# Kernel tuning notes

Measured on AMD Instinct MI355X. Metric: run time of the kernel, lower is better.

The kernel has to match this reference:

```python
import jax, jax.numpy as jnp
import numpy as np

FEW_SHOT_K = 5
NUM_CLASSES = 3
SUPPORT_SIZE = 100


def setup_inputs() -> dict:
    key = jax.random.key(0)
    ks = jax.random.split(key, 12)
    B, S, H = 64, 512, 1024
    scale = 0.02
    return {
        "hidden_states": jax.random.normal(ks[0], (B, S, H), jnp.float32),
        "labels": jax.random.randint(ks[1], (B,), 0, NUM_CLASSES),
        "support_features": jax.random.normal(ks[2], (SUPPORT_SIZE, H), jnp.float32),
        "support_labels": jax.random.randint(ks[3], (SUPPORT_SIZE,), 0, NUM_CLASSES),
        "W_sim": jax.random.normal(ks[4], (128, H), jnp.float32) * scale,
        "b_sim": jnp.zeros((128,), jnp.float32),
        "W_div": jax.random.normal(ks[5], (128, H), jnp.float32) * scale,
        "b_div": jnp.zeros((128,), jnp.float32),
        "W_meta": jax.random.normal(ks[6], (H, H), jnp.float32) * scale,
        "b_meta": jnp.zeros((H,), jnp.float32),
        "W_con": jax.random.normal(ks[7], (256, H), jnp.float32) * scale,
        "b_con": jnp.zeros((256,), jnp.float32),
    }


def reference(hidden_states, labels, support_features, support_labels,
              W_sim, b_sim, W_div, b_div, W_meta, b_meta, W_con, b_con):
    B, S, H = hidden_states.shape
    pooled = hidden_states.mean(axis=1)                       # [B,H] sentence/query features
    similarity_features = pooled @ W_sim.T + b_sim            # [B,128]
    diversity_features = pooled @ W_div.T + b_div             # [B,128]
    meta = jnp.einsum('bsh,oh->bso', hidden_states, W_meta) + b_meta  # [B,S,H]
    meta_contrastive = meta.mean(axis=1) @ W_con.T + b_con    # [B,256]

    # update_support_set: circular buffer write starting at ptr=0, B<100 -> plain slice.
    # Features are .detach()'d in torch before storage.
    supF = support_features.at[:B].set(jax.lax.stop_gradient(pooled))
    supL = support_labels.at[:B].set(labels)

    # topk similarity + softmax weights
    sims = pooled @ supF.T                                    # [B,100]
    top_v, top_i = jax.lax.top_k(sims, FEW_SHOT_K)            # [B,K]
    weights = jax.nn.softmax(top_v, axis=1)                   # [B,K]
    sel_labels = supL[top_i]                                  # [B,K]

    # vectorized replacement of the per-element python scatter loop:
    # pred[b,c] = sum_i weights[b,i] * [sel_labels[b,i] == c], 0<=label<3 guard
    # jax.nn.one_hot yields all-zeros for out-of-range labels, matching the guard.
    onehot = jax.nn.one_hot(sel_labels, NUM_CLASSES, dtype=weights.dtype)  # [B,K,3]
    pred = jnp.einsum('bkc,bk->bc', onehot, weights)          # [B,3]
    few_shot_predictions = jnp.broadcast_to(pred[:, None, :], (B, S, NUM_CLASSES))

    return few_shot_predictions, similarity_features, diversity_features, meta_contrastive
```

## Files before the change

### kernel.cpp

```cpp
#include <hip/hip_runtime.h>

#define BB 64
#define SS 512
#define HH 1024
#define SUP 100
#define KFS 5
#define NCLS 3
#define SEG 32
#define KSPLIT 8
#define KB (HH / KSPLIT)
#define KC 32
#define ASLD 68

__global__ void pool_partial(const float* __restrict__ hs, float* __restrict__ part) {
    int blk = blockIdx.x;
    int b   = blk >> 5;
    int seg = blk & (SEG - 1);
    int t   = threadIdx.x;
    const float4* src = (const float4*)(hs + (size_t)b * SS * HH);
    float4 acc = make_float4(0.f, 0.f, 0.f, 0.f);
    int s0 = seg * (SS / SEG);
#pragma unroll
    for (int s = s0; s < s0 + (SS / SEG); ++s) {
        float4 v = src[s * 256 + t];
        acc.x += v.x; acc.y += v.y; acc.z += v.z; acc.w += v.w;
    }
    ((float4*)part)[(seg * BB + b) * 256 + t] = acc;
}

__global__ void pool_reduce(const float* __restrict__ part, float* __restrict__ pooled) {
    int b = blockIdx.x;
    int t = threadIdx.x;
    float4 acc = make_float4(0.f, 0.f, 0.f, 0.f);
    for (int seg = 0; seg < SEG; ++seg) {
        float4 v = ((const float4*)part)[(seg * BB + b) * 256 + t];
        acc.x += v.x; acc.y += v.y; acc.z += v.z; acc.w += v.w;
    }
    const float inv = 1.0f / 512.0f;
    acc.x *= inv; acc.y *= inv; acc.z *= inv; acc.w *= inv;
    ((float4*)pooled)[b * 256 + t] = acc;
}

__device__ __forceinline__ void gemm64_partial(const float* __restrict__ A,
                                               const float* __restrict__ W,
                                               float* __restrict__ partOut, int N,
                                               int n0, int k0, int ks, int t,
                                               float (*As)[ASLD], float (*Bs)[ASLD]) {
    int tm = t >> 4, tn = t & 15;
    int lr = t >> 2, lq = t & 3;
    float acc[4][4] = {};
    for (int kc = 0; kc < KB; kc += KC) {
        int ka = k0 + kc + lq * 4;
        float4 a0 = *(const float4*)(A + (size_t)lr * HH + ka);
        float4 a1 = *(const float4*)(A + (size_t)lr * HH + ka + 16);
        float4 w0 = *(const float4*)(W + (size_t)(n0 + lr) * HH + ka);
        float4 w1 = *(const float4*)(W + (size_t)(n0 + lr) * HH + ka + 16);
        As[lq * 4 + 0][lr] = a0.x; As[lq * 4 + 1][lr] = a0.y;
        As[lq * 4 + 2][lr] = a0.z; As[lq * 4 + 3][lr] = a0.w;
        As[16 + lq * 4 + 0][lr] = a1.x; As[16 + lq * 4 + 1][lr] = a1.y;
        As[16 + lq * 4 + 2][lr] = a1.z; As[16 + lq * 4 + 3][lr] = a1.w;
        Bs[lq * 4 + 0][lr] = w0.x; Bs[lq * 4 + 1][lr] = w0.y;
        Bs[lq * 4 + 2][lr] = w0.z; Bs[lq * 4 + 3][lr] = w0.w;
        Bs[16 + lq * 4 + 0][lr] = w1.x; Bs[16 + lq * 4 + 1][lr] = w1.y;
        Bs[16 + lq * 4 + 2][lr] = w1.z; Bs[16 + lq * 4 + 3][lr] = w1.w;
        __syncthreads();
#pragma unroll
        for (int k = 0; k < KC; ++k) {
            float4 a4 = *(const float4*)&As[k][tm * 4];
            float4 b4 = *(const float4*)&Bs[k][tn * 4];
            acc[0][0] += a4.x * b4.x; acc[0][1] += a4.x * b4.y;
            acc[0][2] += a4.x * b4.z; acc[0][3] += a4.x * b4.w;
            acc[1][0] += a4.y * b4.x; acc[1][1] += a4.y * b4.y;
            acc[1][2] += a4.y * b4.z; acc[1][3] += a4.y * b4.w;
            acc[2][0] += a4.z * b4.x; acc[2][1] += a4.z * b4.y;
            acc[2][2] += a4.z * b4.z; acc[2][3] += a4.z * b4.w;
            acc[3][0] += a4.w * b4.x; acc[3][1] += a4.w * b4.y;
            acc[3][2] += a4.w * b4.z; acc[3][3] += a4.w * b4.w;
        }
        __syncthreads();
    }
#pragma unroll
    for (int i = 0; i < 4; ++i) {
        float4 o = make_float4(acc[i][0], acc[i][1], acc[i][2], acc[i][3]);
        *(float4*)(partOut + ((size_t)ks * 64 + tm * 4 + i) * N + n0 + tn * 4) = o;
    }
}

__global__ void lin_partial(const float* __restrict__ pooled,
                            const float* __restrict__ W_sim,
                            const float* __restrict__ W_div,
                            const float* __restrict__ W_met,
                            float* __restrict__ pSim, float* __restrict__ pDiv,
                            float* __restrict__ pMet) {
    __shared__ __align__(16) float As[KC][ASLD];
    __shared__ __align__(16) float Bs[KC][ASLD];
    int b = blockIdx.x, t = threadIdx.x;
    if (b < 16) {
        gemm64_partial(pooled, W_sim, pSim, 128, (b >> 3) * 64, (b & 7) * KB, b & 7, t, As, Bs);
    } else if (b < 32) {
        int id = b - 16;
        gemm64_partial(pooled, W_div, pDiv, 128, (id >> 3) * 64, (id & 7) * KB, id & 7, t, As, Bs);
    } else {
        int id = b - 32;
        gemm64_partial(pooled, W_met, pMet, 1024, (id >> 3) * 64, (id & 7) * KB, id & 7, t, As, Bs);
    }
}

__global__ void tail_fewshot_con(const float* __restrict__ pMet,
                                 const float* __restrict__ b_met,
                                 const float* __restrict__ W_con,
                                 float* __restrict__ pCon,
                                 const float* __restrict__ pooled,
                                 const float* __restrict__ supF,
                                 const int* __restrict__ labels,
                                 const int* __restrict__ supL,
                                 float* __restrict__ out_fsp) {
    __shared__ __align__(16) float As[KC][ASLD];
    __shared__ __align__(16) float Bs[KC][ASLD];
    __shared__ float ps[HH];
    __shared__ float sims[SUP];
    __shared__ float pred[NCLS];
    int blk = blockIdx.x, t = threadIdx.x;

    if (blk >= BB) {
        int id = blk - BB;
        int n0 = (id >> 3) * 64, ks = id & 7, k0 = ks * KB;
        int tm = t >> 4, tn = t & 15;
        int lr = t >> 2, lq = t & 3;
        float acc[4][4] = {};
        for (int kc = 0; kc < KB; kc += KC) {
            int ka = k0 + kc + lq * 4;
            float4 s0 = *(const float4*)(b_met + ka);
            float4 s1 = *(const float4*)(b_met + ka + 16);
#pragma unroll
            for (int p = 0; p < KSPLIT; ++p) {
                float4 v0 = *(const float4*)(pMet + ((size_t)p * 64 + lr) * HH + ka);
                float4 v1 = *(const float4*)(pMet + ((size_t)p * 64 + lr) * HH + ka + 16);
                s0.x += v0.x; s0.y += v0.y; s0.z += v0.z; s0.w += v0.w;
                s1.x += v1.x; s1.y += v1.y; s1.z += v1.z; s1.w += v1.w;
            }
            float4 w0 = *(const float4*)(W_con + (size_t)(n0 + lr) * HH + ka);
            float4 w1 = *(const float4*)(W_con + (size_t)(n0 + lr) * HH + ka + 16);
            As[lq * 4 + 0][lr] = s0.x; As[lq * 4 + 1][lr] = s0.y;
            As[lq * 4 + 2][lr] = s0.z; As[lq * 4 + 3][lr] = s0.w;
            As[16 + lq * 4 + 0][lr] = s1.x; As[16 + lq * 4 + 1][lr] = s1.y;
            As[16 + lq * 4 + 2][lr] = s1.z; As[16 + lq * 4 + 3][lr] = s1.w;
            Bs[lq * 4 + 0][lr] = w0.x; Bs[lq * 4 + 1][lr] = w0.y;
            Bs[lq * 4 + 2][lr] = w0.z; Bs[lq * 4 + 3][lr] = w0.w;
            Bs[16 + lq * 4 + 0][lr] = w1.x; Bs[16 + lq * 4 + 1][lr] = w1.y;
            Bs[16 + lq * 4 + 2][lr] = w1.z; Bs[16 + lq * 4 + 3][lr] = w1.w;
            __syncthreads();
#pragma unroll
            for (int k = 0; k < KC; ++k) {
                float4 a4 = *(const float4*)&As[k][tm * 4];
                float4 b4 = *(const float4*)&Bs[k][tn * 4];
                acc[0][0] += a4.x * b4.x; acc[0][1] += a4.x * b4.y;
                acc[0][2] += a4.x * b4.z; acc[0][3] += a4.x * b4.w;
                acc[1][0] += a4.y * b4.x; acc[1][1] += a4.y * b4.y;
                acc[1][2] += a4.y * b4.z; acc[1][3] += a4.y * b4.w;
                acc[2][0] += a4.z * b4.x; acc[2][1] += a4.z * b4.y;
                acc[2][2] += a4.z * b4.z; acc[2][3] += a4.z * b4.w;
                acc[3][0] += a4.w * b4.x; acc[3][1] += a4.w * b4.y;
                acc[3][2] += a4.w * b4.z; acc[3][3] += a4.w * b4.w;
            }
            __syncthreads();
        }
#pragma unroll
        for (int i = 0; i < 4; ++i) {
            float4 o = make_float4(acc[i][0], acc[i][1], acc[i][2], acc[i][3]);
            *(float4*)(pCon + ((size_t)ks * 64 + tm * 4 + i) * 256 + n0 + tn * 4) = o;
        }
        return;
    }

    int b = blk;
    ((float4*)ps)[t] = ((const float4*)(pooled + (size_t)b * HH))[t];
    __syncthreads();

    int wave = t >> 6, lane = t & 63;
    for (int j = wave; j < SUP; j += 4) {
        const float* row = (j < BB) ? (pooled + (size_t)j * HH)
                                    : (supF + (size_t)j * HH);
        float s = 0.f;
#pragma unroll
        for (int q = 0; q < 16; ++q) {
            int h = lane + q * 64;
            s += ps[h] * row[h];
        }
        for (int off = 32; off; off >>= 1) s += __shfl_down(s, off);
        if (lane == 0) sims[j] = s;
    }
    __syncthreads();

    if (t == 0) {
        float vals[KFS]; int idx[KFS];
        for (int i = 0; i < KFS; ++i) {
            float best = -3.4e38f; int bi = 0;
            for (int j = 0; j < SUP; ++j) {
                bool taken = false;
                for (int p = 0; p < i; ++p) taken = taken || (idx[p] == j);
                if (!taken && sims[j] > best) { best = sims[j]; bi = j; }
            }
            vals[i] = best; idx[i] = bi;
        }
        float mx = vals[0];
        for (int i = 1; i < KFS; ++i) mx = fmaxf(mx, vals[i]);
        float e[KFS], sum = 0.f;
        for (int i = 0; i < KFS; ++i) { e[i] = __expf(vals[i] - mx); sum += e[i]; }
        float p0 = 0.f, p1 = 0.f, p2 = 0.f;
        for (int i = 0; i < KFS; ++i) {
            int j = idx[i];
            int lab = (j < BB) ? labels[j] : supL[j];
            float wv = e[i] / sum;
            if (lab == 0) p0 += wv;
            else if (lab == 1) p1 += wv;
            else if (lab == 2) p2 += wv;
        }
        pred[0] = p0; pred[1] = p1; pred[2] = p2;
    }
    __syncthreads();

    float p[NCLS] = {pred[0], pred[1], pred[2]};
    for (int i = t; i < SS * NCLS; i += 256) {
        int c = i - (i / NCLS) * NCLS;
        out_fsp[(size_t)b * SS * NCLS + i] = p[c];
    }
}

__global__ void combine(const float* __restrict__ pSim, const float* __restrict__ b_sim,
                        const float* __restrict__ pDiv, const float* __restrict__ b_div,
                        const float* __restrict__ pCon, const float* __restrict__ b_con,
                        float* __restrict__ out_sim, float* __restrict__ out_div,
                        float* __restrict__ out_con) {
    int gid = blockIdx.x * 256 + threadIdx.x;
    if (gid < 8192) {
        float s = b_sim[gid & 127];
#pragma unroll
        for (int p = 0; p < KSPLIT; ++p) s += pSim[p * 8192 + gid];
        out_sim[gid] = s;
    } else if (gid < 16384) {
        int i = gid - 8192;
        float s = b_div[i & 127];
#pragma unroll
        for (int p = 0; p < KSPLIT; ++p) s += pDiv[p * 8192 + i];
        out_div[i] = s;
    } else {
        int i = gid - 16384;
        float s = b_con[i & 255];
#pragma unroll
        for (int p = 0; p < KSPLIT; ++p) s += pCon[p * 16384 + i];
        out_con[i] = s;
    }
}

extern "C" void kernel_launch(void* const* d_in, const int* in_sizes, int n_in,
                              void* d_out, int out_size, void* d_ws, size_t ws_size,
                              hipStream_t stream) {
    const float* hs    = (const float*)d_in[0];
    const int*   lab   = (const int*)  d_in[1];
    const float* supF  = (const float*)d_in[2];
    const int*   supL  = (const int*)  d_in[3];
    const float* W_sim = (const float*)d_in[4];
    const float* b_sim = (const float*)d_in[5];
    const float* W_div = (const float*)d_in[6];
    const float* b_div = (const float*)d_in[7];
    const float* W_met = (const float*)d_in[8];
    const float* b_met = (const float*)d_in[9];
    const float* W_con = (const float*)d_in[10];
    const float* b_con = (const float*)d_in[11];

    float* out = (float*)d_out;
    float* out_fsp  = out;
    float* out_sim  = out + 98304;
    float* out_div  = out + 106496;
    float* out_con  = out + 114688;

    float* ws     = (float*)d_ws;
    float* part   = ws;
    float* pooled = part + (size_t)SEG * BB * HH;
    float* pSim   = pooled + BB * HH;
    float* pDiv   = pSim + KSPLIT * BB * 128;
    float* pMet   = pDiv + KSPLIT * BB * 128;
    float* pCon   = pMet + (size_t)KSPLIT * BB * HH;

    pool_partial<<<BB * SEG, 256, 0, stream>>>(hs, part);
    pool_reduce <<<BB,       256, 0, stream>>>(part, pooled);
    lin_partial <<<160,      256, 0, stream>>>(pooled, W_sim, W_div, W_met, pSim, pDiv, pMet);
    tail_fewshot_con<<<96,   256, 0, stream>>>(pMet, b_met, W_con, pCon,
                                               pooled, supF, lab, supL, out_fsp);
    combine<<<128, 256, 0, stream>>>(pSim, b_sim, pDiv, b_div, pCon, b_con,
                                     out_sim, out_div, out_con);
}
```

Before: 83.14 us.

## Precompose W_con·W_meta and fuse pipeline into two kernels with flag sync

Uses associativity to precompute W_con@W_meta (256x1024) and the folded bias W_con·b_met in the first kernel, overlapping that weight-only GEMM with the hidden-state pooling. The second kernel fuses pool reduce, few-shot top-k, the sim/div/con GEMMs and the final combine, using global atomic counters with spin-waits instead of separate launches. This removes the large [B,H]x[H,H] meta GEMM and three kernel launches. In exchange it depends on all spinning blocks being co-resident, and it changes the floating-point summation order.

Measured after the change: 127.7 us. 1.54x slower.

```diff
diff --git a/kernel.cpp b/kernel.cpp
--- a/kernel.cpp
+++ b/kernel.cpp
@@ -11,34 +11,93 @@
 #define KB (HH / KSPLIT)
 #define KC 32
 #define ASLD 68
-
-__global__ void pool_partial(const float* __restrict__ hs, float* __restrict__ part) {
-    int blk = blockIdx.x;
-    int b   = blk >> 5;
-    int seg = blk & (SEG - 1);
-    int t   = threadIdx.x;
-    const float4* src = (const float4*)(hs + (size_t)b * SS * HH);
-    float4 acc = make_float4(0.f, 0.f, 0.f, 0.f);
-    int s0 = seg * (SS / SEG);
-#pragma unroll
-    for (int s = s0; s < s0 + (SS / SEG); ++s) {
-        float4 v = src[s * 256 + t];
-        acc.x += v.x; acc.y += v.y; acc.z += v.z; acc.w += v.w;
-    }
-    ((float4*)part)[(seg * BB + b) * 256 + t] = acc;
-}
-
-__global__ void pool_reduce(const float* __restrict__ part, float* __restrict__ pooled) {
-    int b = blockIdx.x;
-    int t = threadIdx.x;
-    float4 acc = make_float4(0.f, 0.f, 0.f, 0.f);
-    for (int seg = 0; seg < SEG; ++seg) {
-        float4 v = ((const float4*)part)[(seg * BB + b) * 256 + t];
-        acc.x += v.x; acc.y += v.y; acc.z += v.z; acc.w += v.w;
-    }
-    const float inv = 1.0f / 512.0f;
-    acc.x *= inv; acc.y *= inv; acc.z *= inv; acc.w *= inv;
-    ((float4*)pooled)[b * 256 + t] = acc;
+#define WKS 4
+#define WKB (HH / WKS)
+
+#define POOL_BLKS (BB * SEG)
+#define WG_BLKS   256
+
+__global__ void k1_pool_wgemm(const float* __restrict__ hs,
+                              const float* __restrict__ W_con,
+                              const float* __restrict__ W_met,
+                              const float* __restrict__ b_met,
+                              const float* __restrict__ b_con,
+                              float* __restrict__ part,
+                              float* __restrict__ pWcm,
+                              float* __restrict__ b_cm,
+                              unsigned int* __restrict__ flags) {
+    int blk = blockIdx.x, t = threadIdx.x;
+
+    if (blk < POOL_BLKS) {
+        int b = blk >> 5, seg = blk & (SEG - 1);
+        const float4* src = (const float4*)(hs + (size_t)b * SS * HH);
+        float4 acc = make_float4(0.f, 0.f, 0.f, 0.f);
+        int s0 = seg * (SS / SEG);
+#pragma unroll
+        for (int s = s0; s < s0 + (SS / SEG); ++s) {
+            float4 v = src[s * 256 + t];
+            acc.x += v.x; acc.y += v.y; acc.z += v.z; acc.w += v.w;
+        }
+        ((float4*)part)[(seg * BB + b) * 256 + t] = acc;
+        return;
+    }
+
+    if (blk < POOL_BLKS + WG_BLKS) {
+        __shared__ __align__(16) float As[KC][ASLD];
+        __shared__ __align__(16) float Bs[KC][ASLD];
+        int id = blk - POOL_BLKS;
+        int p    = id & 3;
+        int tile = id >> 2;
+        int o0 = (tile & 3) * 64;
+        int h0 = (tile >> 2) * 64;
+        int m0 = p * WKB;
+        int tm = t >> 4, tn = t & 15;
+        int lr = t >> 2, lq = t & 3;
+        int mr = t >> 3, hq = t & 7;
+        float acc[4][4] = {};
+        for (int kc = 0; kc < WKB; kc += KC) {
+            int ma = m0 + kc;
+            float4 a0 = *(const float4*)(W_con + (size_t)(o0 + lr) * HH + ma + lq * 4);
+            float4 a1 = *(const float4*)(W_con + (size_t)(o0 + lr) * HH + ma + lq * 4 + 16);
+            As[lq*4+0][lr] = a0.x; As[lq*4+1][lr] = a0.y; As[lq*4+2][lr] = a0.z; As[lq*4+3][lr] = a0.w;
+            As[16+lq*4+0][lr] = a1.x; As[16+lq*4+1][lr] = a1.y; As[16+lq*4+2][lr] = a1.z; As[16+lq*4+3][lr] = a1.w;
+            float4 w0 = *(const float4*)(W_met + (size_t)(ma + mr) * HH + h0 + hq * 4);
+            float4 w1 = *(const float4*)(W_met + (size_t)(ma + mr) * HH + h0 + hq * 4 + 32);
+            *(float4*)&Bs[mr][hq * 4]      = w0;
+            *(float4*)&Bs[mr][hq * 4 + 32] = w1;
+            __syncthreads();
+#pragma unroll
+            for (int k = 0; k < KC; ++k) {
+                float4 a4 = *(const float4*)&As[k][tm * 4];
+                float4 b4 = *(const float4*)&Bs[k][tn * 4];
+                acc[0][0] += a4.x * b4.x; acc[0][1] += a4.x * b4.y;
+                acc[0][2] += a4.x * b4.z; acc[0][3] += a4.x * b4.w;
+                acc[1][0] += a4.y * b4.x; acc[1][1] += a4.y * b4.y;
+                acc[1][2] += a4.y * b4.z; acc[1][3] += a4.y * b4.w;
+                acc[2][0] += a4.z * b4.x; acc[2][1] += a4.z * b4.y;
+                acc[2][2] += a4.z * b4.z; acc[2][3] += a4.z * b4.w;
+                acc[3][0] += a4.w * b4.x; acc[3][1] += a4.w * b4.y;
+                acc[3][2] += a4.w * b4.z; acc[3][3] += a4.w * b4.w;
+            }
+            __syncthreads();
+        }
+#pragma unroll
+        for (int i = 0; i < 4; ++i)
+            *(float4*)(pWcm + ((size_t)p * 256 + o0 + tm * 4 + i) * HH + h0 + tn * 4) =
+                make_float4(acc[i][0], acc[i][1], acc[i][2], acc[i][3]);
+        return;
+    }
+
+    if (t < 2) flags[t] = 0u;
+    float s = b_con[t];
+    const float4* wr  = (const float4*)(W_con + (size_t)t * HH);
+    const float4* bm4 = (const float4*)b_met;
+#pragma unroll 8
+    for (int m = 0; m < HH / 4; ++m) {
+        float4 w = wr[m], bm = bm4[m];
+        s += w.x * bm.x + w.y * bm.y + w.z * bm.z + w.w * bm.w;
+    }
+    b_cm[t] = s;
 }
 
 __device__ __forceinline__ void gemm64_partial(const float* __restrict__ A,
@@ -55,14 +114,10 @@
         float4 a1 = *(const float4*)(A + (size_t)lr * HH + ka + 16);
         float4 w0 = *(const float4*)(W + (size_t)(n0 + lr) * HH + ka);
         float4 w1 = *(const float4*)(W + (size_t)(n0 + lr) * HH + ka + 16);
-        As[lq * 4 + 0][lr] = a0.x; As[lq * 4 + 1][lr] = a0.y;
-        As[lq * 4 + 2][lr] = a0.z; As[lq * 4 + 3][lr] = a0.w;
-        As[16 + lq * 4 + 0][lr] = a1.x; As[16 + lq * 4 + 1][lr] = a1.y;
-        As[16 + lq * 4 + 2][lr] = a1.z; As[16 + lq * 4 + 3][lr] = a1.w;
-        Bs[lq * 4 + 0][lr] = w0.x; Bs[lq * 4 + 1][lr] = w0.y;
-        Bs[lq * 4 + 2][lr] = w0.z; Bs[lq * 4 + 3][lr] = w0.w;
-        Bs[16 + lq * 4 + 0][lr] = w1.x; Bs[16 + lq * 4 + 1][lr] = w1.y;
-        Bs[16 + lq * 4 + 2][lr] = w1.z; Bs[16 + lq * 4 + 3][lr] = w1.w;
+        As[lq*4+0][lr] = a0.x; As[lq*4+1][lr] = a0.y; As[lq*4+2][lr] = a0.z; As[lq*4+3][lr] = a0.w;
+        As[16+lq*4+0][lr] = a1.x; As[16+lq*4+1][lr] = a1.y; As[16+lq*4+2][lr] = a1.z; As[16+lq*4+3][lr] = a1.w;
+        Bs[lq*4+0][lr] = w0.x; Bs[lq*4+1][lr] = w0.y; Bs[lq*4+2][lr] = w0.z; Bs[lq*4+3][lr] = w0.w;
+        Bs[16+lq*4+0][lr] = w1.x; Bs[16+lq*4+1][lr] = w1.y; Bs[16+lq*4+2][lr] = w1.z; Bs[16+lq*4+3][lr] = w1.w;
         __syncthreads();
 #pragma unroll
         for (int k = 0; k < KC; ++k) {
@@ -80,176 +135,195 @@
         __syncthreads();
     }
 #pragma unroll
-    for (int i = 0; i < 4; ++i) {
-        float4 o = make_float4(acc[i][0], acc[i][1], acc[i][2], acc[i][3]);
-        *(float4*)(partOut + ((size_t)ks * 64 + tm * 4 + i) * N + n0 + tn * 4) = o;
-    }
+    for (int i = 0; i < 4; ++i)
+        *(float4*)(partOut + ((size_t)ks * 64 + tm * 4 + i) * N + n0 + tn * 4) =
+            make_float4(acc[i][0], acc[i][1], acc[i][2], acc[i][3]);
 }
 
-__global__ void lin_partial(const float* __restrict__ pooled,
-                            const float* __restrict__ W_sim,
-                            const float* __restrict__ W_div,
-                            const float* __restrict__ W_met,
-                            float* __restrict__ pSim, float* __restrict__ pDiv,
-                            float* __restrict__ pMet) {
-    __shared__ __align__(16) float As[KC][ASLD];
-    __shared__ __align__(16) float Bs[KC][ASLD];
-    int b = blockIdx.x, t = threadIdx.x;
-    if (b < 16) {
-        gemm64_partial(pooled, W_sim, pSim, 128, (b >> 3) * 64, (b & 7) * KB, b & 7, t, As, Bs);
-    } else if (b < 32) {
-        int id = b - 16;
-        gemm64_partial(pooled, W_div, pDiv, 128, (id >> 3) * 64, (id & 7) * KB, id & 7, t, As, Bs);
-    } else {
-        int id = b - 32;
-        gemm64_partial(pooled, W_met, pMet, 1024, (id >> 3) * 64, (id & 7) * KB, id & 7, t, As, Bs);
-    }
-}
-
-__global__ void tail_fewshot_con(const float* __restrict__ pMet,
-                                 const float* __restrict__ b_met,
-                                 const float* __restrict__ W_con,
-                                 float* __restrict__ pCon,
-                                 const float* __restrict__ pooled,
-                                 const float* __restrict__ supF,
-                                 const int* __restrict__ labels,
-                                 const int* __restrict__ supL,
-                                 float* __restrict__ out_fsp) {
+__global__ void __launch_bounds__(256, 2)
+k2_main(const float* __restrict__ part,
+        const float* __restrict__ supF,
+        const int* __restrict__ labels,
+        const int* __restrict__ supL,
+        const float* __restrict__ W_sim, const float* __restrict__ b_sim,
+        const float* __restrict__ W_div, const float* __restrict__ b_div,
+        const float* __restrict__ pWcm,  const float* __restrict__ b_cm,
+        float* __restrict__ pooled,
+        float* __restrict__ pSim, float* __restrict__ pDiv, float* __restrict__ pCon,
+        float* __restrict__ out_fsp, float* __restrict__ out_sim,
+        float* __restrict__ out_div, float* __restrict__ out_con,
+        unsigned int* __restrict__ flags) {
     __shared__ __align__(16) float As[KC][ASLD];
     __shared__ __align__(16) float Bs[KC][ASLD];
     __shared__ float ps[HH];
-    __shared__ float sims[SUP];
+    __shared__ float simsS[SUP];
     __shared__ float pred[NCLS];
     int blk = blockIdx.x, t = threadIdx.x;
 
-    if (blk >= BB) {
+    if (blk < BB) {
+        int b = blk;
+        float4 acc = make_float4(0.f, 0.f, 0.f, 0.f);
+        for (int seg = 0; seg < SEG; ++seg) {
+            float4 v = ((const float4*)part)[(seg * BB + b) * 256 + t];
+            acc.x += v.x; acc.y += v.y; acc.z += v.z; acc.w += v.w;
+        }
+        const float inv = 1.0f / 512.0f;
+        acc.x *= inv; acc.y *= inv; acc.z *= inv; acc.w *= inv;
+        ((float4*)ps)[t] = acc;
+        ((float4*)(pooled + (size_t)b * HH))[t] = acc;
+        __syncthreads();
+        __threadfence();
+        if (t == 0)
+            __hip_atomic_fetch_add(&flags[0], 1u, __ATOMIC_RELEASE, __HIP_MEMORY_SCOPE_AGENT);
+        if (t == 0) {
+            while (__hip_atomic_load(&flags[0], __ATOMIC_ACQUIRE, __HIP_MEMORY_SCOPE_AGENT) < BB)
+                __builtin_amdgcn_s_sleep(2);
+        }
+        __syncthreads();
+        __threadfence();
+
+        int wave = t >> 6, lane = t & 63;
+        for (int j = wave; j < SUP; j += 4) {
+            const float* row = (j < BB) ? (pooled + (size_t)j * HH)
+                                        : (supF + (size_t)j * HH);
+            float s = 0.f;
+#pragma unroll
+            for (int q = 0; q < 16; ++q) {
+                int h = lane + q * 64;
+                s += ps[h] * row[h];
+            }
+            for (int off = 32; off; off >>= 1) s += __shfl_down(s, off);
+            if (lane == 0) simsS[j] = s;
+        }
+        __syncthreads();
+
+        if (t == 0) {
+            float vals[KFS]; int idx[KFS];
+            for (int i = 0; i < KFS; ++i) {
+                float best = -3.4e38f; int bi = 0;
+                for (int j = 0; j < SUP; ++j) {
+                    bool taken = false;
+                    for (int p = 0; p < i; ++p) taken = taken || (idx[p] == j);
+                    if (!taken && simsS[j] > best) { best = simsS[j]; bi = j; }
+                }
+                vals[i] = best; idx[i] = bi;
+            }
+            float mx = vals[0];
+            for (int i = 1; i < KFS; ++i) mx = fmaxf(mx, vals[i]);
+            float e[KFS], sum = 0.f;
+            for (int i = 0; i < KFS; ++i) { e[i] = __expf(vals[i] - mx); sum += e[i]; }
+            float p0 = 0.f, p1 = 0.f, p2 = 0.f;
+            for (int i = 0; i < KFS; ++i) {
+                int j = idx[i];
+                int lab = (j < BB) ? labels[j] : supL[j];
+                float wv = e[i] / sum;
+                if (lab == 0) p0 += wv;
+                else if (lab == 1) p1 += wv;
+                else if (lab == 2) p2 += wv;
+            }
+            pred[0] = p0; pred[1] = p1; pred[2] = p2;
+        }
+        __syncthreads();
+
+        float p[NCLS] = {pred[0], pred[1], pred[2]};
+        for (int i = t; i < SS * NCLS; i += 256) {
+            int c = i - (i / NCLS) * NCLS;
+            out_fsp[(size_t)b * SS * NCLS + i] = p[c];
+        }
+        return;
+    }
+
+    if (blk < 2 * BB) {
+        if (t == 0) {
+            while (__hip_atomic_load(&flags[0], __ATOMIC_ACQUIRE, __HIP_MEMORY_SCOPE_AGENT) < BB)
+                __builtin_amdgcn_s_sleep(2);
+        }
+        __syncthreads();
+        __threadfence();
+
         int id = blk - BB;
-        int n0 = (id >> 3) * 64, ks = id & 7, k0 = ks * KB;
-        int tm = t >> 4, tn = t & 15;
-        int lr = t >> 2, lq = t & 3;
-        float acc[4][4] = {};
-        for (int kc = 0; kc < KB; kc += KC) {
-            int ka = k0 + kc + lq * 4;
-            float4 s0 = *(const float4*)(b_met + ka);
-            float4 s1 = *(const float4*)(b_met + ka + 16);
-#pragma unroll
-            for (int p = 0; p < KSPLIT; ++p) {
-                float4 v0 = *(const float4*)(pMet + ((size_t)p * 64 + lr) * HH + ka);
-                float4 v1 = *(const float4*)(pMet + ((size_t)p * 64 + lr) * HH + ka + 16);
-                s0.x += v0.x; s0.y += v0.y; s0.z += v0.z; s0.w += v0.w;
-                s1.x += v1.x; s1.y += v1.y; s1.z += v1.z; s1.w += v1.w;
-            }
-            float4 w0 = *(const float4*)(W_con + (size_t)(n0 + lr) * HH + ka);
-            float4 w1 = *(const float4*)(W_con + (size_t)(n0 + lr) * HH + ka + 16);
-            As[lq * 4 + 0][lr] = s0.x; As[lq * 4 + 1][lr] = s0.y;
-            As[lq * 4 + 2][lr] = s0.z; As[lq * 4 + 3][lr] = s0.w;
-            As[16 + lq * 4 + 0][lr] = s1.x; As[16 + lq * 4 + 1][lr] = s1.y;
-            As[16 + lq * 4 + 2][lr] = s1.z; As[16 + lq * 4 + 3][lr] = s1.w;
-            Bs[lq * 4 + 0][lr] = w0.x; Bs[lq * 4 + 1][lr] = w0.y;
-            Bs[lq * 4 + 2][lr] = w0.z; Bs[lq * 4 + 3][lr] = w0.w;
-            Bs[16 + lq * 4 + 0][lr] = w1.x; Bs[16 + lq * 4 + 1][lr] = w1.y;
-            Bs[16 + lq * 4 + 2][lr] = w1.z; Bs[16 + lq * 4 + 3][lr] = w1.w;
-            __syncthreads();
-#pragma unroll
-            for (int k = 0; k < KC; ++k) {
-                float4 a4 = *(const float4*)&As[k][tm * 4];
-                float4 b4 = *(const float4*)&Bs[k][tn * 4];
-                acc[0][0] += a4.x * b4.x; acc[0][1] += a4.x * b4.y;
-                acc[0][2] += a4.x * b4.z; acc[0][3] += a4.x * b4.w;
-                acc[1][0] += a4.y * b4.x; acc[1][1] += a4.y * b4.y;
-                acc[1][2] += a4.y * b4.z; acc[1][3] += a4.y * b4.w;
-                acc[2][0] += a4.z * b4.x; acc[2][1] += a4.z * b4.y;
-                acc[2][2] += a4.z * b4.z; acc[2][3] += a4.z * b4.w;
-                acc[3][0] += a4.w * b4.x; acc[3][1] += a4.w * b4.y;
-                acc[3][2] += a4.w * b4.z; acc[3][3] += a4.w * b4.w;
-            }
-            __syncthreads();
-        }
-#pragma unroll
-        for (int i = 0; i < 4; ++i) {
-            float4 o = make_float4(acc[i][0], acc[i][1], acc[i][2], acc[i][3]);
-            *(float4*)(pCon + ((size_t)ks * 64 + tm * 4 + i) * 256 + n0 + tn * 4) = o;
-        }
+        if (id < 16) {
+            gemm64_partial(pooled, W_sim, pSim, 128, (id >> 3) * 64, (id & 7) * KB, id & 7, t, As, Bs);
+        } else if (id < 32) {
+            int i2 = id - 16;
+            gemm64_partial(pooled, W_div, pDiv, 128, (i2 >> 3) * 64, (i2 & 7) * KB, i2 & 7, t, As, Bs);
+        } else {
+            int i2 = id - 32;
+            int n0 = (i2 >> 3) * 64, ks = i2 & 7, k0 = ks * KB;
+            int tm = t >> 4, tn = t & 15;
+            int lr = t >> 2, lq = t & 3;
+            float acc[4][4] = {};
+            for (int kc = 0; kc < KB; kc += KC) {
+                int ka = k0 + kc + lq * 4;
+                float4 a0 = *(const float4*)(pooled + (size_t)lr * HH + ka);
+                float4 a1 = *(const float4*)(pooled + (size_t)lr * HH + ka + 16);
+                float4 w0 = make_float4(0.f, 0.f, 0.f, 0.f), w1 = w0;
+#pragma unroll
+                for (int p = 0; p < WKS; ++p) {
+                    float4 v0 = *(const float4*)(pWcm + ((size_t)p * 256 + n0 + lr) * HH + ka);
+                    float4 v1 = *(const float4*)(pWcm + ((size_t)p * 256 + n0 + lr) * HH + ka + 16);
+                    w0.x += v0.x; w0.y += v0.y; w0.z += v0.z; w0.w += v0.w;
+                    w1.x += v1.x; w1.y += v1.y; w1.z += v1.z; w1.w += v1.w;
+                }
+                As[lq*4+0][lr] = a0.x; As[lq*4+1][lr] = a0.y; As[lq*4+2][lr] = a0.z; As[lq*4+3][lr] = a0.w;
+                As[16+lq*4+0][lr] = a1.x; As[16+lq*4+1][lr] = a1.y; As[16+lq*4+2][lr] = a1.z; As[16+lq*4+3][lr] = a1.w;
+                Bs[lq*4+0][lr] = w0.x; Bs[lq*4+1][lr] = w0.y; Bs[lq*4+2][lr] = w0.z; Bs[lq*4+3][lr] = w0.w;
+                Bs[16+lq*4+0][lr] = w1.x; Bs[16+lq*4+1][lr] = w1.y; Bs[16+lq*4+2][lr] = w1.z; Bs[16+lq*4+3][lr] = w1.w;
+                __syncthreads();
+#pragma unroll
+                for (int k = 0; k < KC; ++k) {
+                    float4 a4 = *(const float4*)&As[k][tm * 4];
+                    float4 b4 = *(const float4*)&Bs[k][tn * 4];
+                    acc[0][0] += a4.x * b4.x; acc[0][1] += a4.x * b4.y;
+                    acc[0][2] += a4.x * b4.z; acc[0][3] += a4.x * b4.w;
+                    acc[1][0] += a4.y * b4.x; acc[1][1] += a4.y * b4.y;
+                    acc[1][2] += a4.y * b4.z; acc[1][3] += a4.y * b4.w;
+                    acc[2][0] += a4.z * b4.x; acc[2][1] += a4.z * b4.y;
+                    acc[2][2] += a4.z * b4.z; acc[2][3] += a4.z * b4.w;
+                    acc[3][0] += a4.w * b4.x; acc[3][1] += a4.w * b4.y;
+                    acc[3][2] += a4.w * b4.z; acc[3][3] += a4.w * b4.w;
+                }
+                __syncthreads();
+            }
+#pragma unroll
+            for (int i = 0; i < 4; ++i)
+                *(float4*)(pCon + ((size_t)ks * 64 + tm * 4 + i) * 256 + n0 + tn * 4) =
+                    make_float4(acc[i][0], acc[i][1], acc[i][2], acc[i][3]);
+        }
+        __syncthreads();
+        __threadfence();
+        if (t == 0)
+            __hip_atomic_fetch_add(&flags[1], 1u, __ATOMIC_RELEASE, __HIP_MEMORY_SCOPE_AGENT);
         return;
     }
 
-    int b = blk;
-    ((float4*)ps)[t] = ((const float4*)(pooled + (size_t)b * HH))[t];
+    if (t == 0) {
+        while (__hip_atomic_load(&flags[1], __ATOMIC_ACQUIRE, __HIP_MEMORY_SCOPE_AGENT) < BB)
+            __builtin_amdgcn_s_sleep(2);
+    }
     __syncthreads();
-
-    int wave = t >> 6, lane = t & 63;
-    for (int j = wave; j < SUP; j += 4) {
-        const float* row = (j < BB) ? (pooled + (size_t)j * HH)
-                                    : (supF + (size_t)j * HH);
-        float s = 0.f;
-#pragma unroll
-        for (int q = 0; q < 16; ++q) {
-            int h = lane + q * 64;
-            s += ps[h] * row[h];
-        }
-        for (int off = 32; off; off >>= 1) s += __shfl_down(s, off);
-        if (lane == 0) sims[j] = s;
-    }
-    __syncthreads();
-
-    if (t == 0) {
-        float vals[KFS]; int idx[KFS];
-        for (int i = 0; i < KFS; ++i) {
-            float best = -3.4e38f; int bi = 0;
-            for (int j = 0; j < SUP; ++j) {
-                bool taken = false;
-                for (int p = 0; p < i; ++p) taken = taken || (idx[p] == j);
-                if (!taken && sims[j] > best) { best = sims[j]; bi = j; }
-            }
-            vals[i] = best; idx[i] = bi;
-        }
-        float mx = vals[0];
-        for (int i = 1; i < KFS; ++i) mx = fmaxf(mx, vals[i]);
-        float e[KFS], sum = 0.f;
-        for (int i = 0; i < KFS; ++i) { e[i] = __expf(vals[i] - mx); sum += e[i]; }
-        float p0 = 0.f, p1 = 0.f, p2 = 0.f;
-        for (int i = 0; i < KFS; ++i) {
-            int j = idx[i];
-            int lab = (j < BB) ? labels[j] : supL[j];
-            float wv = e[i] / sum;
-            if (lab == 0) p0 += wv;
-            else if (lab == 1) p1 += wv;
-            else if (lab == 2) p2 += wv;
-        }
-        pred[0] = p0; pred[1] = p1; pred[2] = p2;
-    }
-    __syncthreads();
-
-    float p[NCLS] = {pred[0], pred[1], pred[2]};
-    for (int i = t; i < SS * NCLS; i += 256) {
-        int c = i - (i / NCLS) * NCLS;
-        out_fsp[(size_t)b * SS * NCLS + i] = p[c];
-    }
-}
-
-__global__ void combine(const float* __restrict__ pSim, const float* __restrict__ b_sim,
-                        const float* __restrict__ pDiv, const float* __restrict__ b_div,
-                        const float* __restrict__ pCon, const float* __restrict__ b_con,
-                        float* __restrict__ out_sim, float* __restrict__ out_div,
-                        float* __restrict__ out_con) {
-    int gid = blockIdx.x * 256 + threadIdx.x;
-    if (gid < 8192) {
-        float s = b_sim[gid & 127];
-#pragma unroll
-        for (int p = 0; p < KSPLIT; ++p) s += pSim[p * 8192 + gid];
-        out_sim[gid] = s;
-    } else if (gid < 16384) {
-        int i = gid - 8192;
-        float s = b_div[i & 127];
-#pragma unroll
-        for (int p = 0; p < KSPLIT; ++p) s += pDiv[p * 8192 + i];
-        out_div[i] = s;
-    } else {
-        int i = gid - 16384;
-        float s = b_con[i & 255];
-#pragma unroll
-        for (int p = 0; p < KSPLIT; ++p) s += pCon[p * 16384 + i];
-        out_con[i] = s;
+    __threadfence();
+
+    int gid = (blk - 2 * BB) * 256 + t;
+    for (int i = gid; i < 32768; i += 2048) {
+        if (i < 8192) {
+            float s = b_sim[i & 127];
+#pragma unroll
+            for (int p = 0; p < KSPLIT; ++p) s += pSim[p * 8192 + i];
+            out_sim[i] = s;
+        } else if (i < 16384) {
+            int i2 = i - 8192;
+            float s = b_div[i2 & 127];
+#pragma unroll
+            for (int p = 0; p < KSPLIT; ++p) s += pDiv[p * 8192 + i2];
+            out_div[i2] = s;
+        } else {
+            int i2 = i - 16384;
+            float s = b_cm[i2 & 255];
+#pragma unroll
+            for (int p = 0; p < KSPLIT; ++p) s += pCon[p * 16384 + i2];
+            out_con[i2] = s;
+        }
     }
 }
 
@@ -270,24 +344,25 @@
     const float* b_con = (const float*)d_in[11];
 
     float* out = (float*)d_out;
-    float* out_fsp  = out;
-    float* out_sim  = out + 98304;
-    float* out_div  = out + 106496;
-    float* out_con  = out + 114688;
+    float* out_fsp = out;
+    float* out_sim = out + 98304;
+    float* out_div = out + 106496;
+    float* out_con = out + 114688;
 
     float* ws     = (float*)d_ws;
     float* part   = ws;
     float* pooled = part + (size_t)SEG * BB * HH;
-    float* pSim   = pooled + BB * HH;
+    float* pWcm   = pooled + BB * HH;
+    float* b_cm   = pWcm + (size_t)WKS * 256 * HH;
+    float* pSim   = b_cm + 256;
     float* pDiv   = pSim + KSPLIT * BB * 128;
-    float* pMet   = pDiv + KSPLIT * BB * 128;
-    float* pCon   = pMet + (size_t)KSPLIT * BB * HH;
-
-    pool_partial<<<BB * SEG, 256, 0, stream>>>(hs, part);
-    pool_reduce <<<BB,       256, 0, stream>>>(part, pooled);
-    lin_partial <<<160,      256, 0, stream>>>(pooled, W_sim, W_div, W_met, pSim, pDiv, pMet);
-    tail_fewshot_con<<<96,   256, 0, stream>>>(pMet, b_met, W_con, pCon,
-                                               pooled, supF, lab, supL, out_fsp);
-    combine<<<128, 256, 0, stream>>>(pSim, b_sim, pDiv, b_div, pCon, b_con,
-                                     out_sim, out_div, out_con);
+    float* pCon   = pDiv + KSPLIT * BB * 128;
+    unsigned int* flags = (unsigned int*)(pCon + KSPLIT * BB * 256);
+
+    k1_pool_wgemm<<<POOL_BLKS + WG_BLKS + 1, 256, 0, stream>>>(
+        hs, W_con, W_met, b_met, b_con, part, pWcm, b_cm, flags);
+
+    k2_main<<<2 * BB + 8, 256, 0, stream>>>(
+        part, supF, lab, supL, W_sim, b_sim, W_div, b_div, pWcm, b_cm,
+        pooled, pSim, pDiv, pCon, out_fsp, out_sim, out_div, out_con, flags);
 }
```

## Move few-shot similarity GEMM into linear-partial kernel and batch pooled loads

Applied to the files above, without the earlier changes.

The pooled-versus-support similarity matrix is now computed as an extra split-K tiled GEMM inside lin_partial (16 extra blocks), rather than by 64 blocks each doing serial wave dot products in the tail kernel. The tail kernel then only reduces the partial sims before its top-k. The aim is to shorten the critical path of the tail kernel and reuse pooled rows across batch items. Separately, pool_partial issues all 16 loads up front and sums them as a tree to expose more memory-level parallelism. The cost is extra workspace traffic for the partial sims and clamped, wasted rows beyond the 100 support entries.

New measurement: 69.64 us. 1.19x faster.

```diff
diff --git a/kernel.cpp b/kernel.cpp
--- a/kernel.cpp
+++ b/kernel.cpp
@@ -17,23 +17,27 @@
     int b   = blk >> 5;
     int seg = blk & (SEG - 1);
     int t   = threadIdx.x;
-    const float4* src = (const float4*)(hs + (size_t)b * SS * HH);
-    float4 acc = make_float4(0.f, 0.f, 0.f, 0.f);
-    int s0 = seg * (SS / SEG);
-#pragma unroll
-    for (int s = s0; s < s0 + (SS / SEG); ++s) {
-        float4 v = src[s * 256 + t];
-        acc.x += v.x; acc.y += v.y; acc.z += v.z; acc.w += v.w;
-    }
-    ((float4*)part)[(seg * BB + b) * 256 + t] = acc;
+    const float4* src = (const float4*)(hs + (size_t)b * SS * HH) + (size_t)(seg * 16) * 256 + t;
+    float4 v[16];
+#pragma unroll
+    for (int i = 0; i < 16; ++i) v[i] = src[(size_t)i * 256];
+#pragma unroll
+    for (int st = 8; st; st >>= 1)
+#pragma unroll
+        for (int i = 0; i < st; ++i) {
+            v[i].x += v[i + st].x; v[i].y += v[i + st].y;
+            v[i].z += v[i + st].z; v[i].w += v[i + st].w;
+        }
+    ((float4*)part)[(size_t)(seg * BB + b) * 256 + t] = v[0];
 }
 
 __global__ void pool_reduce(const float* __restrict__ part, float* __restrict__ pooled) {
     int b = blockIdx.x;
     int t = threadIdx.x;
     float4 acc = make_float4(0.f, 0.f, 0.f, 0.f);
+#pragma unroll 4
     for (int seg = 0; seg < SEG; ++seg) {
-        float4 v = ((const float4*)part)[(seg * BB + b) * 256 + t];
+        float4 v = ((const float4*)part)[(size_t)(seg * BB + b) * 256 + t];
         acc.x += v.x; acc.y += v.y; acc.z += v.z; acc.w += v.w;
     }
     const float inv = 1.0f / 512.0f;
@@ -55,14 +59,10 @@
         float4 a1 = *(const float4*)(A + (size_t)lr * HH + ka + 16);
         float4 w0 = *(const float4*)(W + (size_t)(n0 + lr) * HH + ka);
         float4 w1 = *(const float4*)(W + (size_t)(n0 + lr) * HH + ka + 16);
-        As[lq * 4 + 0][lr] = a0.x; As[lq * 4 + 1][lr] = a0.y;
-        As[lq * 4 + 2][lr] = a0.z; As[lq * 4 + 3][lr] = a0.w;
-        As[16 + lq * 4 + 0][lr] = a1.x; As[16 + lq * 4 + 1][lr] = a1.y;
-        As[16 + lq * 4 + 2][lr] = a1.z; As[16 + lq * 4 + 3][lr] = a1.w;
-        Bs[lq * 4 + 0][lr] = w0.x; Bs[lq * 4 + 1][lr] = w0.y;
-        Bs[lq * 4 + 2][lr] = w0.z; Bs[lq * 4 + 3][lr] = w0.w;
-        Bs[16 + lq * 4 + 0][lr] = w1.x; Bs[16 + lq * 4 + 1][lr] = w1.y;
-        Bs[16 + lq * 4 + 2][lr] = w1.z; Bs[16 + lq * 4 + 3][lr] = w1.w;
+        As[lq*4+0][lr] = a0.x; As[lq*4+1][lr] = a0.y; As[lq*4+2][lr] = a0.z; As[lq*4+3][lr] = a0.w;
+        As[16+lq*4+0][lr] = a1.x; As[16+lq*4+1][lr] = a1.y; As[16+lq*4+2][lr] = a1.z; As[16+lq*4+3][lr] = a1.w;
+        Bs[lq*4+0][lr] = w0.x; Bs[lq*4+1][lr] = w0.y; Bs[lq*4+2][lr] = w0.z; Bs[lq*4+3][lr] = w0.w;
+        Bs[16+lq*4+0][lr] = w1.x; Bs[16+lq*4+1][lr] = w1.y; Bs[16+lq*4+2][lr] = w1.z; Bs[16+lq*4+3][lr] = w1.w;
         __syncthreads();
 #pragma unroll
         for (int k = 0; k < KC; ++k) {
@@ -80,75 +80,56 @@
         __syncthreads();
     }
 #pragma unroll
-    for (int i = 0; i < 4; ++i) {
-        float4 o = make_float4(acc[i][0], acc[i][1], acc[i][2], acc[i][3]);
-        *(float4*)(partOut + ((size_t)ks * 64 + tm * 4 + i) * N + n0 + tn * 4) = o;
-    }
+    for (int i = 0; i < 4; ++i)
+        *(float4*)(partOut + ((size_t)ks * 64 + tm * 4 + i) * N + n0 + tn * 4) =
+            make_float4(acc[i][0], acc[i][1], acc[i][2], acc[i][3]);
 }
 
 __global__ void lin_partial(const float* __restrict__ pooled,
                             const float* __restrict__ W_sim,
                             const float* __restrict__ W_div,
                             const float* __restrict__ W_met,
+                            const float* __restrict__ supF,
                             float* __restrict__ pSim, float* __restrict__ pDiv,
-                            float* __restrict__ pMet) {
+                            float* __restrict__ pMet, float* __restrict__ pSims) {
     __shared__ __align__(16) float As[KC][ASLD];
     __shared__ __align__(16) float Bs[KC][ASLD];
-    int b = blockIdx.x, t = threadIdx.x;
-    if (b < 16) {
-        gemm64_partial(pooled, W_sim, pSim, 128, (b >> 3) * 64, (b & 7) * KB, b & 7, t, As, Bs);
-    } else if (b < 32) {
-        int id = b - 16;
-        gemm64_partial(pooled, W_div, pDiv, 128, (id >> 3) * 64, (id & 7) * KB, id & 7, t, As, Bs);
-    } else {
-        int id = b - 32;
-        gemm64_partial(pooled, W_met, pMet, 1024, (id >> 3) * 64, (id & 7) * KB, id & 7, t, As, Bs);
-    }
-}
-
-__global__ void tail_fewshot_con(const float* __restrict__ pMet,
-                                 const float* __restrict__ b_met,
-                                 const float* __restrict__ W_con,
-                                 float* __restrict__ pCon,
-                                 const float* __restrict__ pooled,
-                                 const float* __restrict__ supF,
-                                 const int* __restrict__ labels,
-                                 const int* __restrict__ supL,
-                                 float* __restrict__ out_fsp) {
-    __shared__ __align__(16) float As[KC][ASLD];
-    __shared__ __align__(16) float Bs[KC][ASLD];
-    __shared__ float ps[HH];
-    __shared__ float sims[SUP];
-    __shared__ float pred[NCLS];
-    int blk = blockIdx.x, t = threadIdx.x;
-
-    if (blk >= BB) {
-        int id = blk - BB;
-        int n0 = (id >> 3) * 64, ks = id & 7, k0 = ks * KB;
+    int id = blockIdx.x, t = threadIdx.x;
+
+    if (id < 16) {
+        gemm64_partial(pooled, W_sim, pSim, 128, (id >> 3) * 64, (id & 7) * KB, id & 7, t, As, Bs);
+        return;
+    }
+    if (id < 32) {
+        int i2 = id - 16;
+        gemm64_partial(pooled, W_div, pDiv, 128, (i2 >> 3) * 64, (i2 & 7) * KB, i2 & 7, t, As, Bs);
+        return;
+    }
+    if (id < 160) {
+        int i2 = id - 32;
+        gemm64_partial(pooled, W_met, pMet, 1024, (i2 >> 3) * 64, (i2 & 7) * KB, i2 & 7, t, As, Bs);
+        return;
+    }
+
+    {
+        int i2 = id - 160;
+        int n0 = (i2 >> 3) * 64, ks = i2 & 7, k0 = ks * KB;
         int tm = t >> 4, tn = t & 15;
         int lr = t >> 2, lq = t & 3;
         float acc[4][4] = {};
+        int j = n0 + lr;
+        const float* wrow = (j < BB) ? (pooled + (size_t)j * HH)
+                                     : (supF + (size_t)(j < SUP ? j : SUP - 1) * HH);
         for (int kc = 0; kc < KB; kc += KC) {
             int ka = k0 + kc + lq * 4;
-            float4 s0 = *(const float4*)(b_met + ka);
-            float4 s1 = *(const float4*)(b_met + ka + 16);
-#pragma unroll
-            for (int p = 0; p < KSPLIT; ++p) {
-                float4 v0 = *(const float4*)(pMet + ((size_t)p * 64 + lr) * HH + ka);
-                float4 v1 = *(const float4*)(pMet + ((size_t)p * 64 + lr) * HH + ka + 16);
-                s0.x += v0.x; s0.y += v0.y; s0.z += v0.z; s0.w += v0.w;
-                s1.x += v1.x; s1.y += v1.y; s1.z += v1.z; s1.w += v1.w;
-            }
-            float4 w0 = *(const float4*)(W_con + (size_t)(n0 + lr) * HH + ka);
-            float4 w1 = *(const float4*)(W_con + (size_t)(n0 + lr) * HH + ka + 16);
-            As[lq * 4 + 0][lr] = s0.x; As[lq * 4 + 1][lr] = s0.y;
-            As[lq * 4 + 2][lr] = s0.z; As[lq * 4 + 3][lr] = s0.w;
-            As[16 + lq * 4 + 0][lr] = s1.x; As[16 + lq * 4 + 1][lr] = s1.y;
-            As[16 + lq * 4 + 2][lr] = s1.z; As[16 + lq * 4 + 3][lr] = s1.w;
-            Bs[lq * 4 + 0][lr] = w0.x; Bs[lq * 4 + 1][lr] = w0.y;
-            Bs[lq * 4 + 2][lr] = w0.z; Bs[lq * 4 + 3][lr] = w0.w;
-            Bs[16 + lq * 4 + 0][lr] = w1.x; Bs[16 + lq * 4 + 1][lr] = w1.y;
-            Bs[16 + lq * 4 + 2][lr] = w1.z; Bs[16 + lq * 4 + 3][lr] = w1.w;
+            float4 a0 = *(const float4*)(pooled + (size_t)lr * HH + ka);
+            float4 a1 = *(const float4*)(pooled + (size_t)lr * HH + ka + 16);
+            float4 w0 = *(const float4*)(wrow + ka);
+            float4 w1 = *(const float4*)(wrow + ka + 16);
+            As[lq*4+0][lr] = a0.x; As[lq*4+1][lr] = a0.y; As[lq*4+2][lr] = a0.z; As[lq*4+3][lr] = a0.w;
+            As[16+lq*4+0][lr] = a1.x; As[16+lq*4+1][lr] = a1.y; As[16+lq*4+2][lr] = a1.z; As[16+lq*4+3][lr] = a1.w;
+            Bs[lq*4+0][lr] = w0.x; Bs[lq*4+1][lr] = w0.y; Bs[lq*4+2][lr] = w0.z; Bs[lq*4+3][lr] = w0.w;
+            Bs[16+lq*4+0][lr] = w1.x; Bs[16+lq*4+1][lr] = w1.y; Bs[16+lq*4+2][lr] = w1.z; Bs[16+lq*4+3][lr] = w1.w;
             __syncthreads();
 #pragma unroll
             for (int k = 0; k < KC; ++k) {
@@ -166,29 +147,79 @@
             __syncthreads();
         }
 #pragma unroll
-        for (int i = 0; i < 4; ++i) {
-            float4 o = make_float4(acc[i][0], acc[i][1], acc[i][2], acc[i][3]);
-            *(float4*)(pCon + ((size_t)ks * 64 + tm * 4 + i) * 256 + n0 + tn * 4) = o;
-        }
+        for (int i = 0; i < 4; ++i)
+            *(float4*)(pSims + ((size_t)ks * 64 + tm * 4 + i) * 128 + n0 + tn * 4) =
+                make_float4(acc[i][0], acc[i][1], acc[i][2], acc[i][3]);
+    }
+}
+
+__global__ void k4_tail(const float* __restrict__ pSims,
+                        const int* __restrict__ labels,
+                        const int* __restrict__ supL,
+                        const float* __restrict__ pMet,
+                        const float* __restrict__ b_met,
+                        const float* __restrict__ W_con,
+                        float* __restrict__ pCon,
+                        float* __restrict__ out_fsp) {
+    __shared__ __align__(16) float As[KC][ASLD];
+    __shared__ __align__(16) float Bs[KC][ASLD];
+    __shared__ float simsS[128];
+    __shared__ float pred[NCLS];
+    int blk = blockIdx.x, t = threadIdx.x;
+
+    if (blk >= BB) {
+        int id = blk - BB;
+        int n0 = (id >> 3) * 64, ks = id & 7, k0 = ks * KB;
+        int tm = t >> 4, tn = t & 15;
+        int lr = t >> 2, lq = t & 3;
+        float acc[4][4] = {};
+        for (int kc = 0; kc < KB; kc += KC) {
+            int ka = k0 + kc + lq * 4;
+            float4 s0 = *(const float4*)(b_met + ka);
+            float4 s1 = *(const float4*)(b_met + ka + 16);
+#pragma unroll
+            for (int p = 0; p < KSPLIT; ++p) {
+                float4 v0 = *(const float4*)(pMet + ((size_t)p * 64 + lr) * HH + ka);
+                float4 v1 = *(const float4*)(pMet + ((size_t)p * 64 + lr) * HH + ka + 16);
+                s0.x += v0.x; s0.y += v0.y; s0.z += v0.z; s0.w += v0.w;
+                s1.x += v1.x; s1.y += v1.y; s1.z += v1.z; s1.w += v1.w;
+            }
+            float4 w0 = *(const float4*)(W_con + (size_t)(n0 + lr) * HH + ka);
+            float4 w1 = *(const float4*)(W_con + (size_t)(n0 + lr) * HH + ka + 16);
+            As[lq*4+0][lr] = s0.x; As[lq*4+1][lr] = s0.y; As[lq*4+2][lr] = s0.z; As[lq*4+3][lr] = s0.w;
+            As[16+lq*4+0][lr] = s1.x; As[16+lq*4+1][lr] = s1.y; As[16+lq*4+2][lr] = s1.z; As[16+lq*4+3][lr] = s1.w;
+            Bs[lq*4+0][lr] = w0.x; Bs[lq*4+1][lr] = w0.y; Bs[lq*4+2][lr] = w0.z; Bs[lq*4+3][lr] = w0.w;
+            Bs[16+lq*4+0][lr] = w1.x; Bs[16+lq*4+1][lr] = w1.y; Bs[16+lq*4+2][lr] = w1.z; Bs[16+lq*4+3][lr] = w1.w;
+            __syncthreads();
+#pragma unroll
+            for (int k = 0; k < KC; ++k) {
+                float4 a4 = *(const float4*)&As[k][tm * 4];
+                float4 b4 = *(const float4*)&Bs[k][tn * 4];
+                acc[0][0] += a4.x * b4.x; acc[0][1] += a4.x * b4.y;
+                acc[0][2] += a4.x * b4.z; acc[0][3] += a4.x * b4.w;
+                acc[1][0] += a4.y * b4.x; acc[1][1] += a4.y * b4.y;
+                acc[1][2] += a4.y * b4.z; acc[1][3] += a4.y * b4.w;
+                acc[2][0] += a4.z * b4.x; acc[2][1] += a4.z * b4.y;
+                acc[2][2] += a4.z * b4.z; acc[2][3] += a4.z * b4.w;
+                acc[3][0] += a4.w * b4.x; acc[3][1] += a4.w * b4.y;
+                acc[3][2] += a4.w * b4.z; acc[3][3] += a4.w * b4.w;
+            }
+            __syncthreads();
+        }
+#pragma unroll
+        for (int i = 0; i < 4; ++i)
+            *(float4*)(pCon + ((size_t)ks * 64 + tm * 4 + i) * 256 + n0 + tn * 4) =
+                make_float4(acc[i][0], acc[i][1], acc[i][2], acc[i][3]);
         return;
     }
 
     int b = blk;
-    ((float4*)ps)[t] = ((const float4*)(pooled + (size_t)b * HH))[t];
-    __syncthreads();
-
-    int wave = t >> 6, lane = t & 63;
-    for (int j = wave; j < SUP; j += 4) {
-        const float* row = (j < BB) ? (pooled + (size_t)j * HH)
-                                    : (supF + (size_t)j * HH);
+    if (t < 128) {
         float s = 0.f;
 #pragma unroll
-        for (int q = 0; q < 16; ++q) {
-            int h = lane + q * 64;
-            s += ps[h] * row[h];
-        }
-        for (int off = 32; off; off >>= 1) s += __shfl_down(s, off);
-        if (lane == 0) sims[j] = s;
+        for (int ks = 0; ks < KSPLIT; ++ks)
+            s += pSims[((size_t)ks * 64 + b) * 128 + t];
+        simsS[t] = s;
     }
     __syncthreads();
 
@@ -199,7 +230,7 @@
             for (int j = 0; j < SUP; ++j) {
                 bool taken = false;
                 for (int p = 0; p < i; ++p) taken = taken || (idx[p] == j);
-                if (!taken && sims[j] > best) { best = sims[j]; bi = j; }
+                if (!taken && simsS[j] > best) { best = simsS[j]; bi = j; }
             }
             vals[i] = best; idx[i] = bi;
         }
@@ -270,10 +301,10 @@
     const float* b_con = (const float*)d_in[11];
 
     float* out = (float*)d_out;
-    float* out_fsp  = out;
-    float* out_sim  = out + 98304;
-    float* out_div  = out + 106496;
-    float* out_con  = out + 114688;
+    float* out_fsp = out;
+    float* out_sim = out + 98304;
+    float* out_div = out + 106496;
+    float* out_con = out + 114688;
 
     float* ws     = (float*)d_ws;
     float* part   = ws;
@@ -282,12 +313,14 @@
     float* pDiv   = pSim + KSPLIT * BB * 128;
     float* pMet   = pDiv + KSPLIT * BB * 128;
     float* pCon   = pMet + (size_t)KSPLIT * BB * HH;
+    float* pSims  = pCon + KSPLIT * BB * 256;
 
     pool_partial<<<BB * SEG, 256, 0, stream>>>(hs, part);
     pool_reduce <<<BB,       256, 0, stream>>>(part, pooled);
-    lin_partial <<<160,      256, 0, stream>>>(pooled, W_sim, W_div, W_met, pSim, pDiv, pMet);
-    tail_fewshot_con<<<96,   256, 0, stream>>>(pMet, b_met, W_con, pCon,
-                                               pooled, supF, lab, supL, out_fsp);
-    combine<<<128, 256, 0, stream>>>(pSim, b_sim, pDiv, b_div, pCon, b_con,
-                                     out_sim, out_div, out_con);
-}
+    lin_partial <<<176,      256, 0, stream>>>(pooled, W_sim, W_div, W_met, supF,
+                                               pSim, pDiv, pMet, pSims);
+    k4_tail     <<<96,       256, 0, stream>>>(pSims, lab, supL, pMet, b_met, W_con,
+                                               pCon, out_fsp);
+    combine     <<<128,      256, 0, stream>>>(pSim, b_sim, pDiv, b_div, pCon, b_con,
+                                               out_sim, out_div, out_con);
+}
```
